# Kernel optimization log

Hardware: AMD Instinct MI355X
Metric: run time of the kernel (lower is better)

Reference implementation:

```python
import jax, jax.numpy as jnp
import numpy as np

B, C_IN, C_OUT = 16, 256, 128
V_RAW, N_VERT, K = 10242, 40962, 7


def setup_inputs() -> dict:
    key = jax.random.key(0)
    k1, k2, k3, k4, k5, k6 = jax.random.split(key, 6)
    x = jax.random.normal(k1, (B, C_IN, V_RAW), dtype=jnp.float32)
    W = jax.random.normal(k2, (C_OUT, C_IN), dtype=jnp.float32) * (1.0 / np.sqrt(C_IN))
    b = jax.random.normal(k3, (C_OUT,), dtype=jnp.float32) * 0.01
    up_neigh_indices = jax.random.randint(k4, (N_VERT, K), 0, N_VERT, dtype=jnp.int64)
    down_indices = jax.random.randint(k5, (V_RAW,), 0, N_VERT, dtype=jnp.int64)
    max_pool_indices = jax.random.randint(k6, (B, C_OUT, V_RAW), 0, K, dtype=jnp.int64)
    return {"x": x, "W": W, "b": b,
            "up_neigh_indices": up_neigh_indices,
            "down_indices": down_indices,
            "max_pool_indices": max_pool_indices}


def _feats_indices(n_feats: int, n_raw_vertices: int) -> np.ndarray:
    # torch: floor(linspace(0, n_feats, num=n_raw_vertices*n_feats)); last -= 1
    fi = np.floor(np.linspace(0.0, float(n_feats), num=n_raw_vertices * n_feats))
    fi[-1] -= 1
    return fi.astype(np.int64)


def reference(x, W, b, up_neigh_indices, down_indices, max_pool_indices):
    n_samples, in_feats, n_raw = x.shape
    n_vertices = up_neigh_indices.shape[0]
    out_feats = W.shape[0]

    # per-vertex linear projection: (B, Cin, V) -> (B, Cout, V)
    h = jnp.einsum('bcv,oc->bov', x, W) + b[None, :, None]

    # neighbor table at coarse vertices: (V_raw, K)
    neigh = up_neigh_indices[down_indices]

    # vertices_indices[b, f, v] = neigh[v, max_pool_indices[b, f, v]]
    vi = neigh[jnp.arange(n_raw)[None, None, :], max_pool_indices]  # (B, Cout, V_raw)

    # flatten exactly like torch (row-major over (Cout, V_raw))
    h_flat = h.reshape(n_samples, out_feats * n_raw)
    vi_flat = vi.reshape(n_samples, out_feats * n_raw)
    fi = jnp.asarray(_feats_indices(out_feats, n_raw))  # (Cout*V_raw,) static

    y = jnp.zeros((n_samples, out_feats, n_vertices), dtype=h.dtype)
    y = y.at[jnp.arange(n_samples)[:, None], fi[None, :], vi_flat].set(h_flat)
    return y
```

## Files before the change

### kernel.cpp

```cpp
#include <hip/hip_runtime.h>

#define NB    16
#define CIN   256
#define COUT  128
#define VRAW  10242
#define NVERT 40962
#define NPAIR (VRAW * 7)
#define CAP   16
#define LDV   132

typedef __attribute__((ext_vector_type(8))) short short8;
typedef __attribute__((ext_vector_type(4))) short short4v;
typedef __attribute__((ext_vector_type(4))) float floatx4;

__device__ inline unsigned short f2bf(float f) {
    unsigned u = __builtin_bit_cast(unsigned, f);
    u += 0x7fffu + ((u >> 16) & 1u);
    return (unsigned short)(u >> 16);
}

__global__ __launch_bounds__(256) void convw_kernel(const float* __restrict__ W,
                                                    unsigned short* __restrict__ Wbf) {
    int i = blockIdx.x * 256 + threadIdx.x;
    Wbf[i] = f2bf(W[i]);
}

__global__ __launch_bounds__(256) void build_kernel(const int* __restrict__ up,
                                                    const int* __restrict__ down,
                                                    int* __restrict__ cnt,
                                                    unsigned* __restrict__ buckets) {
    int i = blockIdx.x * 256 + threadIdx.x;
    if (i >= NPAIR) return;
    int v = i / 7;
    int k = i - v * 7;
    int t = up[down[v] * 7 + k];
    int pos = atomicAdd(&cnt[t], 1);
    if (pos < CAP) buckets[(size_t)pos * NVERT + t] = ((unsigned)v << 3) | (unsigned)k;
}

__global__ __launch_bounds__(256) void gemm_kernel(const float* __restrict__ x,
                                                   const unsigned short* __restrict__ Wbf,
                                                   const float* __restrict__ bias,
                                                   float* __restrict__ h) {
    __shared__ unsigned short xs[32 * LDV];
    const int b    = blockIdx.y;
    const int v0   = blockIdx.x * 128;
    const int tid  = threadIdx.x;
    const int wave = tid >> 6;
    const int lane = tid & 63;
    const int mn   = lane & 15;
    const int q    = lane >> 4;
    const int vw   = wave * 32;

    const int sc = tid >> 4;
    const int sv = (tid & 15) * 8;
    const bool fullTile = (v0 + 128 <= VRAW);

    floatx4 acc[8][2];
#pragma unroll
    for (int ot = 0; ot < 8; ot++) { acc[ot][0] = (floatx4)0.f; acc[ot][1] = (floatx4)0.f; }

    for (int ck = 0; ck < 8; ck++) {
        const int c0 = ck * 32;
        __syncthreads();
#pragma unroll
        for (int p = 0; p < 2; p++) {
            const int c = p * 16 + sc;
            const float* src = x + ((size_t)(b * CIN + c0 + c)) * VRAW + v0 + sv;
            float f[8];
            if (fullTile) {
#pragma unroll
                for (int u = 0; u < 4; u++) {
                    float2 tt = *(const float2*)(src + 2 * u);
                    f[2 * u] = tt.x; f[2 * u + 1] = tt.y;
                }
            } else {
#pragma unroll
                for (int u = 0; u < 8; u++) {
                    int v = v0 + sv + u;
                    f[u] = (v < VRAW) ? src[u] : 0.f;
                }
            }
            short4v lo, hi;
#pragma unroll
            for (int u = 0; u < 4; u++) { lo[u] = (short)f2bf(f[u]); hi[u] = (short)f2bf(f[4 + u]); }
            unsigned short* dst = &xs[c * LDV + sv];
            *(short4v*)dst = lo;
            *(short4v*)(dst + 4) = hi;
        }
        __syncthreads();

        short8 bfrag[2];
#pragma unroll
        for (int vt = 0; vt < 2; vt++) {
            const int vloc = vw + vt * 16 + mn;
#pragma unroll
            for (int j = 0; j < 8; j++)
                bfrag[vt][j] = (short)xs[(q * 8 + j) * LDV + vloc];
        }
#pragma unroll
        for (int ot = 0; ot < 8; ot++) {
            short8 afrag = *(const short8*)(Wbf + (ot * 16 + mn) * CIN + c0 + q * 8);
            acc[ot][0] = __builtin_amdgcn_mfma_f32_16x16x32_bf16(afrag, bfrag[0], acc[ot][0], 0, 0, 0);
            acc[ot][1] = __builtin_amdgcn_mfma_f32_16x16x32_bf16(afrag, bfrag[1], acc[ot][1], 0, 0, 0);
        }
    }

#pragma unroll
    for (int ot = 0; ot < 8; ot++) {
#pragma unroll
        for (int vt = 0; vt < 2; vt++) {
            const int v = v0 + vw + vt * 16 + mn;
            if (v < VRAW) {
#pragma unroll
                for (int r = 0; r < 4; r++) {
                    const int o = ot * 16 + q * 4 + r;
                    h[((size_t)b * COUT + o) * VRAW + v] = acc[ot][vt][r] + bias[o];
                }
            }
        }
    }
}

__global__ __launch_bounds__(1024) void gather_kernel(const int* __restrict__ cnt,
                                                      const unsigned* __restrict__ buckets,
                                                      const int* __restrict__ mpi,
                                                      const float* __restrict__ h,
                                                      float* __restrict__ y) {
    __shared__ unsigned short mpis[VRAW];
    __shared__ float hs[VRAW];
    const int r   = blockIdx.x;
    const int tid = threadIdx.x;

    const int*   mpiRow = mpi + (size_t)r * VRAW;
    const float* hRow   = h   + (size_t)r * VRAW;
    for (int i = tid; i < VRAW; i += 1024) {
        mpis[i] = (unsigned short)mpiRow[i];
        hs[i]   = hRow[i];
    }
    __syncthreads();

    float* yRow = y + (size_t)r * NVERT;
    for (int t = tid; t < NVERT; t += 1024) {
        int n = cnt[t];
        if (n > CAP) n = CAP;
        int best = -1;
        for (int j = 0; j < n; j++) {
            const unsigned e = buckets[(size_t)j * NVERT + t];
            const int v = (int)(e >> 3);
            const int k = (int)(e & 7u);
            if ((int)mpis[v] == k && v > best) best = v;
        }
        yRow[t] = (best >= 0) ? hs[best] : 0.0f;
    }
}

extern "C" void kernel_launch(void* const* d_in, const int* in_sizes, int n_in,
                              void* d_out, int out_size, void* d_ws, size_t ws_size,
                              hipStream_t stream) {
    const float* x    = (const float*)d_in[0];
    const float* W    = (const float*)d_in[1];
    const float* bias = (const float*)d_in[2];
    const int*   up   = (const int*)d_in[3];
    const int*   down = (const int*)d_in[4];
    const int*   mpi  = (const int*)d_in[5];
    float* y = (float*)d_out;

    char* ws = (char*)d_ws;
    unsigned short* Wbf = (unsigned short*)ws;
    int*      cnt     = (int*)(ws + 65536);
    unsigned* buckets = (unsigned*)(ws + 65536 + 163904);
    float*    h       = (float*)(ws + 65536 + 163904 + (size_t)CAP * NVERT * 4);

    convw_kernel<<<COUT * CIN / 256, 256, 0, stream>>>(W, Wbf);

    hipMemsetAsync(cnt, 0, NVERT * sizeof(int), stream);
    build_kernel<<<(NPAIR + 255) / 256, 256, 0, stream>>>(up, down, cnt, buckets);

    dim3 ggrid((VRAW + 127) / 128, NB);
    gemm_kernel<<<ggrid, 256, 0, stream>>>(x, Wbf, bias, h);

    gather_kernel<<<NB * COUT, 1024, 0, stream>>>(cnt, buckets, mpi, h, y);
}
```

Baseline: 816.1 us.

## Pack per-target buckets contiguously with overflow list; double-buffer GEMM LDS tiles

The scatter table changes from a strided CAP-by-NVERT bucket array into a packed 8-word record per target: a count plus up to seven entries, with a global overflow list for anything beyond that. The gather reads each record with two 16-byte loads, handles two targets per thread, and scans the overflow list only when a wave needs it. The GEMM stages x into double-buffered, vertex-major LDS, so B fragments come from one vector load and the next chunk's global loads overlap the MFMAs. If the overflow list is large, its serial scan could become costly, and overflow beyond OVFCAP is silently dropped.

```diff
diff --git a/kernel.cpp b/kernel.cpp
--- a/kernel.cpp
+++ b/kernel.cpp
@@ -6,11 +6,10 @@
 #define VRAW  10242
 #define NVERT 40962
 #define NPAIR (VRAW * 7)
-#define CAP   16
-#define LDV   132
+#define OVFCAP 8192
+#define LDS_S 40
 
 typedef __attribute__((ext_vector_type(8))) short short8;
-typedef __attribute__((ext_vector_type(4))) short short4v;
 typedef __attribute__((ext_vector_type(4))) float floatx4;
 
 __device__ inline unsigned short f2bf(float f) {
@@ -27,22 +26,31 @@
 
 __global__ __launch_bounds__(256) void build_kernel(const int* __restrict__ up,
                                                     const int* __restrict__ down,
-                                                    int* __restrict__ cnt,
-                                                    unsigned* __restrict__ buckets) {
+                                                    unsigned* __restrict__ packed,
+                                                    unsigned* __restrict__ ovf_cnt,
+                                                    unsigned* __restrict__ ovf) {
     int i = blockIdx.x * 256 + threadIdx.x;
     if (i >= NPAIR) return;
     int v = i / 7;
     int k = i - v * 7;
     int t = up[down[v] * 7 + k];
-    int pos = atomicAdd(&cnt[t], 1);
-    if (pos < CAP) buckets[(size_t)pos * NVERT + t] = ((unsigned)v << 3) | (unsigned)k;
+    unsigned pos = atomicAdd(&packed[(size_t)t * 8], 1u);
+    if (pos < 7u) {
+        packed[(size_t)t * 8 + 1 + pos] = ((unsigned)v << 3) | (unsigned)k;
+    } else {
+        unsigned idx = atomicAdd(ovf_cnt, 1u);
+        if (idx < OVFCAP) {
+            ovf[2 * idx]     = ((unsigned)t << 3) | (unsigned)k;
+            ovf[2 * idx + 1] = (unsigned)v;
+        }
+    }
 }
 
 __global__ __launch_bounds__(256) void gemm_kernel(const float* __restrict__ x,
                                                    const unsigned short* __restrict__ Wbf,
                                                    const float* __restrict__ bias,
                                                    float* __restrict__ h) {
-    __shared__ unsigned short xs[32 * LDV];
+    __shared__ unsigned short xs[2][128 * LDS_S];
     const int b    = blockIdx.y;
     const int v0   = blockIdx.x * 128;
     const int tid  = threadIdx.x;
@@ -51,53 +59,52 @@
     const int mn   = lane & 15;
     const int q    = lane >> 4;
     const int vw   = wave * 32;
-
-    const int sc = tid >> 4;
-    const int sv = (tid & 15) * 8;
-    const bool fullTile = (v0 + 128 <= VRAW);
+    const int cp   = tid >> 4;
+    const int l    = tid & 15;
+    const bool full = (v0 + 128 <= VRAW);
 
     floatx4 acc[8][2];
 #pragma unroll
     for (int ot = 0; ot < 8; ot++) { acc[ot][0] = (floatx4)0.f; acc[ot][1] = (floatx4)0.f; }
 
+    float f0[8], f1[8];
+    auto load_regs = [&](int ck) {
+        const int c0 = ck * 32;
+        const float* p0 = x + ((size_t)(b * CIN + c0 + 2 * cp)) * VRAW + v0 + l;
+        const float* p1 = p0 + VRAW;
+        if (full) {
+#pragma unroll
+            for (int u = 0; u < 8; u++) { f0[u] = p0[16 * u]; f1[u] = p1[16 * u]; }
+        } else {
+#pragma unroll
+            for (int u = 0; u < 8; u++) {
+                const bool ok = (v0 + l + 16 * u) < VRAW;
+                f0[u] = ok ? p0[16 * u] : 0.f;
+                f1[u] = ok ? p1[16 * u] : 0.f;
+            }
+        }
+    };
+    auto write_lds = [&](int buf) {
+        unsigned short* base = xs[buf];
+#pragma unroll
+        for (int u = 0; u < 8; u++) {
+            const int v = l + 16 * u;
+            const unsigned pk = (unsigned)f2bf(f0[u]) | ((unsigned)f2bf(f1[u]) << 16);
+            *(unsigned*)(base + v * LDS_S + 2 * cp) = pk;
+        }
+    };
+
+    load_regs(0);
     for (int ck = 0; ck < 8; ck++) {
+        write_lds(ck & 1);
+        __syncthreads();
+        if (ck < 7) load_regs(ck + 1);
         const int c0 = ck * 32;
-        __syncthreads();
-#pragma unroll
-        for (int p = 0; p < 2; p++) {
-            const int c = p * 16 + sc;
-            const float* src = x + ((size_t)(b * CIN + c0 + c)) * VRAW + v0 + sv;
-            float f[8];
-            if (fullTile) {
-#pragma unroll
-                for (int u = 0; u < 4; u++) {
-                    float2 tt = *(const float2*)(src + 2 * u);
-                    f[2 * u] = tt.x; f[2 * u + 1] = tt.y;
-                }
-            } else {
-#pragma unroll
-                for (int u = 0; u < 8; u++) {
-                    int v = v0 + sv + u;
-                    f[u] = (v < VRAW) ? src[u] : 0.f;
-                }
-            }
-            short4v lo, hi;
-#pragma unroll
-            for (int u = 0; u < 4; u++) { lo[u] = (short)f2bf(f[u]); hi[u] = (short)f2bf(f[4 + u]); }
-            unsigned short* dst = &xs[c * LDV + sv];
-            *(short4v*)dst = lo;
-            *(short4v*)(dst + 4) = hi;
-        }
-        __syncthreads();
-
+        const unsigned short* xb = xs[ck & 1];
         short8 bfrag[2];
 #pragma unroll
-        for (int vt = 0; vt < 2; vt++) {
-            const int vloc = vw + vt * 16 + mn;
-#pragma unroll
-            for (int j = 0; j < 8; j++)
-                bfrag[vt][j] = (short)xs[(q * 8 + j) * LDV + vloc];
-        }
+        for (int vt = 0; vt < 2; vt++)
+            bfrag[vt] = *(const short8*)(xb + (vw + vt * 16 + mn) * LDS_S + q * 8);
 #pragma unroll
         for (int ot = 0; ot < 8; ot++) {
             short8 afrag = *(const short8*)(Wbf + (ot * 16 + mn) * CIN + c0 + q * 8);
@@ -122,8 +129,25 @@
     }
 }
 
-__global__ __launch_bounds__(1024) void gather_kernel(const int* __restrict__ cnt,
-                                                      const unsigned* __restrict__ buckets,
+__device__ inline void probe_t(int t, const unsigned* __restrict__ packed,
+                               const unsigned short* mpis, int& n, int& best) {
+    const uint4 w0 = *(const uint4*)(packed + (size_t)t * 8);
+    const uint4 w1 = *(const uint4*)(packed + (size_t)t * 8 + 4);
+    n = (int)w0.x;
+    unsigned e[7] = {w0.y, w0.z, w0.w, w1.x, w1.y, w1.z, w1.w};
+    best = -1;
+#pragma unroll
+    for (int j = 0; j < 7; j++) {
+        const int v  = (int)(e[j] >> 3);
+        const int k  = (int)(e[j] & 7u);
+        const int vv = v < VRAW ? v : 0;
+        if (j < n && (int)mpis[vv] == k && v > best) best = v;
+    }
+}
+
+__global__ __launch_bounds__(1024) void gather_kernel(const unsigned* __restrict__ packed,
+                                                      const unsigned* __restrict__ ovf_cnt,
+                                                      const unsigned* __restrict__ ovf,
                                                       const int* __restrict__ mpi,
                                                       const float* __restrict__ h,
                                                       float* __restrict__ y) {
@@ -140,18 +164,26 @@
     }
     __syncthreads();
 
+    const int novf = min((int)*ovf_cnt, OVFCAP);
     float* yRow = y + (size_t)r * NVERT;
-    for (int t = tid; t < NVERT; t += 1024) {
-        int n = cnt[t];
-        if (n > CAP) n = CAP;
-        int best = -1;
-        for (int j = 0; j < n; j++) {
-            const unsigned e = buckets[(size_t)j * NVERT + t];
-            const int v = (int)(e >> 3);
-            const int k = (int)(e & 7u);
-            if ((int)mpis[v] == k && v > best) best = v;
-        }
-        yRow[t] = (best >= 0) ? hs[best] : 0.0f;
+
+    for (int t0 = tid; t0 < NVERT; t0 += 2048) {
+        const int t1 = t0 + 1024;
+        int n0, best0, n1 = 0, best1 = -1;
+        probe_t(t0, packed, mpis, n0, best0);
+        if (t1 < NVERT) probe_t(t1, packed, mpis, n1, best1);
+        if (__any(n0 > 7 || n1 > 7)) {
+            for (int i = 0; i < novf; i++) {
+                const unsigned a = ovf[2 * i];
+                const int      vb = (int)ovf[2 * i + 1];
+                const int      tt = (int)(a >> 3);
+                const int      kk = (int)(a & 7u);
+                if (n0 > 7 && tt == t0 && (int)mpis[vb] == kk && vb > best0) best0 = vb;
+                if (n1 > 7 && tt == t1 && (int)mpis[vb] == kk && vb > best1) best1 = vb;
+            }
+        }
+        yRow[t0] = (best0 >= 0) ? hs[best0] : 0.0f;
+        if (t1 < NVERT) yRow[t1] = (best1 >= 0) ? hs[best1] : 0.0f;
     }
 }
 
@@ -167,18 +199,20 @@
     float* y = (float*)d_out;
 
     char* ws = (char*)d_ws;
-    unsigned short* Wbf = (unsigned short*)ws;
-    int*      cnt     = (int*)(ws + 65536);
-    unsigned* buckets = (unsigned*)(ws + 65536 + 163904);
-    float*    h       = (float*)(ws + 65536 + 163904 + (size_t)CAP * NVERT * 4);
+    unsigned short* Wbf     = (unsigned short*)ws;
+    unsigned*       packed  = (unsigned*)(ws + 65536);
+    const size_t packed_sz  = (size_t)NVERT * 8 * 4;
+    unsigned*       ovf_cnt = (unsigned*)(ws + 65536 + packed_sz);
+    unsigned*       ovf     = (unsigned*)(ws + 65536 + packed_sz + 64);
+    float*          h       = (float*)(ws + 65536 + packed_sz + 64 + (size_t)OVFCAP * 8);
+
+    hipMemsetAsync(packed, 0, packed_sz + 64, stream);
 
     convw_kernel<<<COUT * CIN / 256, 256, 0, stream>>>(W, Wbf);
-
-    hipMemsetAsync(cnt, 0, NVERT * sizeof(int), stream);
-    build_kernel<<<(NPAIR + 255) / 256, 256, 0, stream>>>(up, down, cnt, buckets);
+    build_kernel<<<(NPAIR + 255) / 256, 256, 0, stream>>>(up, down, packed, ovf_cnt, ovf);
 
     dim3 ggrid((VRAW + 127) / 128, NB);
     gemm_kernel<<<ggrid, 256, 0, stream>>>(x, Wbf, bias, h);
 
-    gather_kernel<<<NB * COUT, 1024, 0, stream>>>(cnt, buckets, mpi, h, y);
-}
+    gather_kernel<<<NB * COUT, 1024, 0, stream>>>(packed, ovf_cnt, ovf, mpi, h, y);
+}
```

Result: slower. 1.316 ms (+61.2%).
